# Kernel optimization log

Measured on AMD Instinct MI355X. Metric: run time of the kernel, lower is better.

## Reference

```python
import jax, jax.numpy as jnp
import numpy as np

GAMMA = 0.25  # channel_gamma


def q_shift(x, h, w, gamma=GAMMA):
    # x: [B, T, C] with T == h*w; shift 4 channel groups by 1 pixel in 4 directions
    B, T, C = x.shape
    xi = x.reshape(B, h, w, C)
    c = int(C * gamma)
    g0 = jnp.pad(xi[:, :, :-1, 0:c],        ((0, 0), (0, 0), (1, 0), (0, 0)))  # right
    g1 = jnp.pad(xi[:, :, 1:, c:2 * c],     ((0, 0), (0, 0), (0, 1), (0, 0)))  # left
    g2 = jnp.pad(xi[:, :-1, :, 2 * c:3 * c], ((0, 0), (1, 0), (0, 0), (0, 0)))  # down
    g3 = jnp.pad(xi[:, 1:, :, 3 * c:4 * c],  ((0, 0), (0, 1), (0, 0), (0, 0)))  # up
    rest = xi[:, :, :, 4 * c:]
    return jnp.concatenate([g0, g1, g2, g3, rest], axis=-1).reshape(B, T, C)


def wkv(w_dec, u, k, v):
    # Numerically-stabilized RWKV WKV recurrence.
    # w_dec, u: [C]; k, v: [B, T, C] -> y: [B, T, C]
    B, T, C = k.shape
    kT = jnp.transpose(k, (1, 0, 2))  # [T, B, C]
    vT = jnp.transpose(v, (1, 0, 2))

    def step(carry, kv_t):
        p, q, o = carry  # running num/den and log-scale, each [B, C]
        kt, vt = kv_t
        no = jnp.maximum(o, u + kt)
        A = jnp.exp(o - no)
        Bf = jnp.exp(u + kt - no)
        y = (A * p + Bf * vt) / (A * q + Bf)
        no2 = jnp.maximum(w_dec + o, kt)
        A2 = jnp.exp(w_dec + o - no2)
        B2 = jnp.exp(kt - no2)
        return (A2 * p + B2 * vt, A2 * q + B2, no2), y

    init = (jnp.zeros((B, C), k.dtype), jnp.zeros((B, C), k.dtype),
            jnp.full((B, C), -1e38, k.dtype))
    _, yT = jax.lax.scan(step, init, (kT, vT))
    return jnp.transpose(yT, (1, 0, 2))


def layer_norm(x, g, b, eps=1e-5):
    mu = jnp.mean(x, axis=-1, keepdims=True)
    var = jnp.var(x, axis=-1, keepdims=True)
    return (x - mu) * jax.lax.rsqrt(var + eps) * g + b


def setup_inputs() -> dict:
    key = jax.random.key(0)
    ks = jax.random.split(key, 12)
    B, H, W, C = 16, 32, 32, 768
    T = H * W
    x = jax.random.normal(ks[0], (B, T, C), dtype=jnp.float32)
    return {
        "x": x,
        "h": H,
        "w": W,
        "spatial_decay": jax.random.normal(ks[1], (C,), jnp.float32) * 0.5,
        "spatial_first": jax.random.normal(ks[2], (C,), jnp.float32) * 0.5,
        "mix_k": jax.random.uniform(ks[3], (1, 1, C), jnp.float32),
        "mix_v": jax.random.uniform(ks[4], (1, 1, C), jnp.float32),
        "mix_r": jax.random.uniform(ks[5], (1, 1, C), jnp.float32),
        "W_k": jax.random.normal(ks[6], (C, C), jnp.float32) * 0.02,
        "W_v": jax.random.normal(ks[7], (C, C), jnp.float32) * 0.02,
        "W_r": jax.random.normal(ks[8], (C, C), jnp.float32) * 0.02,
        "W_o": jax.random.normal(ks[9], (C, C), jnp.float32) * 0.02,
        "ln_g": jnp.ones((C,), jnp.float32),
        "ln_b": jnp.zeros((C,), jnp.float32),
    }


def reference(x, h, w, spatial_decay, spatial_first, mix_k, mix_v, mix_r,
              W_k, W_v, W_r, W_o, ln_g, ln_b):
    B, T, C = x.shape
    xx = q_shift(x, h, w)
    xk = x * mix_k + xx * (1.0 - mix_k)
    xv = x * mix_v + xx * (1.0 - mix_v)
    xr = x * mix_r + xx * (1.0 - mix_r)
    k = xk @ W_k          # [B, T, C]
    v = xv @ W_v
    sr = jax.nn.sigmoid(xr @ W_r)
    y = wkv(spatial_decay / T, spatial_first / T, k, v)
    y = layer_norm(y, ln_g, ln_b)
    return (sr * y) @ W_o
```

## Files before the change

kernel.cpp:

```cpp
#include <hip/hip_runtime.h>
#include <hip/hip_bf16.h>

using bf16 = __hip_bfloat16;
typedef __attribute__((ext_vector_type(8))) __bf16 bf16x8;
typedef __attribute__((ext_vector_type(4))) float floatx4;

#define B_  16
#define T_  1024
#define C_  768
#define M_  16384

#define OFF_XK ((size_t)0)
#define OFF_XV ((size_t)25165824)
#define OFF_XR ((size_t)50331648)
#define OFF_K  ((size_t)75497472)
#define OFF_V  ((size_t)100663296)
#define OFF_SR ((size_t)125829120)
#define OFF_WT ((size_t)150994944)
#define OFF_Y  ((size_t)0)
#define OFF_Z  ((size_t)50331648)

struct __align__(16) BV8 { bf16 v[8]; };

__global__ __launch_bounds__(256) void transpose_w(
    const float* __restrict__ w0, const float* __restrict__ w1,
    const float* __restrict__ w2, const float* __restrict__ w3,
    bf16* __restrict__ wt) {
  __shared__ float tile[32][33];
  int which = blockIdx.z;
  const float* src = which == 0 ? w0 : which == 1 ? w1 : which == 2 ? w2 : w3;
  bf16* dst = wt + (size_t)which * (C_ * C_);
  int k0 = blockIdx.y * 32;
  int n0 = blockIdx.x * 32;
  int j  = threadIdx.x & 31;
  int i0 = threadIdx.x >> 5;
#pragma unroll
  for (int s = 0; s < 4; s++) {
    int i = i0 + s * 8;
    tile[i][j] = src[(size_t)(k0 + i) * C_ + n0 + j];
  }
  __syncthreads();
#pragma unroll
  for (int s = 0; s < 4; s++) {
    int i = i0 + s * 8;
    dst[(size_t)(n0 + i) * C_ + k0 + j] = __float2bfloat16(tile[j][i]);
  }
}

__global__ __launch_bounds__(256) void shift_mix(
    const float* __restrict__ x,
    const float* __restrict__ mk, const float* __restrict__ mv, const float* __restrict__ mr,
    bf16* __restrict__ xk, bf16* __restrict__ xv, bf16* __restrict__ xr) {
  int gid = blockIdx.x * 256 + threadIdx.x;
  int c8 = gid % 96;
  int bt = gid / 96;
  int b  = bt >> 10;
  int t  = bt & 1023;
  int hh = t >> 5, ww = t & 31;
  int c0 = c8 * 8;
  int g  = c8 / 24;
  int sh = hh, sw = ww;
  bool valid;
  if (g == 0)      { sw = ww - 1; valid = (ww >= 1);  }
  else if (g == 1) { sw = ww + 1; valid = (ww <= 30); }
  else if (g == 2) { sh = hh - 1; valid = (hh >= 1);  }
  else             { sh = hh + 1; valid = (hh <= 30); }
  size_t off = (size_t)bt * C_ + c0;
  float xs[8], ss[8];
  *(float4*)(xs)     = *(const float4*)(x + off);
  *(float4*)(xs + 4) = *(const float4*)(x + off + 4);
  if (valid) {
    size_t soff = (size_t)(b * 1024 + sh * 32 + sw) * C_ + c0;
    *(float4*)(ss)     = *(const float4*)(x + soff);
    *(float4*)(ss + 4) = *(const float4*)(x + soff + 4);
  } else {
#pragma unroll
    for (int j = 0; j < 8; j++) ss[j] = 0.f;
  }
  BV8 ok, ov, orr;
#pragma unroll
  for (int j = 0; j < 8; j++) {
    float xf = xs[j], sf = ss[j];
    float a  = mk[c0 + j];
    float bm = mv[c0 + j];
    float cm = mr[c0 + j];
    ok.v[j]  = __float2bfloat16(xf * a  + sf * (1.f - a));
    ov.v[j]  = __float2bfloat16(xf * bm + sf * (1.f - bm));
    orr.v[j] = __float2bfloat16(xf * cm + sf * (1.f - cm));
  }
  *(BV8*)(xk + off) = ok;
  *(BV8*)(xv + off) = ov;
  *(BV8*)(xr + off) = orr;
}

template <int MODE>
__device__ __forceinline__ void gemm_body(
    const bf16* __restrict__ A, const bf16* __restrict__ BT,
    void* __restrict__ Cout, int M, int N, int K,
    int bx, int by) {
  __shared__ bf16 As[128 * 64];
  __shared__ bf16 Bs[128 * 64];
  int tid  = threadIdx.x;
  int wave = tid >> 6, lane = tid & 63;
  int wm = (wave & 1) * 64, wn = (wave >> 1) * 64;
  size_t m0 = (size_t)by * 128, n0 = (size_t)bx * 128;

  floatx4 acc[4][4];
#pragma unroll
  for (int i = 0; i < 4; i++)
#pragma unroll
    for (int j = 0; j < 4; j++) acc[i][j] = (floatx4){0.f, 0.f, 0.f, 0.f};

  int srow[4], skk[4];
#pragma unroll
  for (int i = 0; i < 4; i++) {
    srow[i] = ((tid >> 2) + i * 64) & 127;
    skk[i]  = (tid & 3) * 8 + (i >> 1) * 32;
  }
  bf16* lA = As + tid * 8;
  bf16* lB = Bs + tid * 8;
  int fr  = lane & 15;
  int fko = (lane >> 4) * 8;

  for (int k0 = 0; k0 < K; k0 += 64) {
#pragma unroll
    for (int i = 0; i < 4; i++) {
      __builtin_amdgcn_global_load_lds(
          (const __attribute__((address_space(1))) void*)(A + (m0 + srow[i]) * (size_t)K + k0 + skk[i]),
          (__attribute__((address_space(3))) void*)(lA + i * 2048), 16, 0, 0);
      __builtin_amdgcn_global_load_lds(
          (const __attribute__((address_space(1))) void*)(BT + (n0 + srow[i]) * (size_t)K + k0 + skk[i]),
          (__attribute__((address_space(3))) void*)(lB + i * 2048), 16, 0, 0);
    }
    __syncthreads();
#pragma unroll
    for (int s = 0; s < 2; s++) {
      bf16x8 af[4], bfr[4];
#pragma unroll
      for (int mi = 0; mi < 4; mi++)
        af[mi] = *(const bf16x8*)(As + s * 4096 + (wm + mi * 16 + fr) * 32 + fko);
#pragma unroll
      for (int ni = 0; ni < 4; ni++)
        bfr[ni] = *(const bf16x8*)(Bs + s * 4096 + (wn + ni * 16 + fr) * 32 + fko);
#pragma unroll
      for (int mi = 0; mi < 4; mi++)
#pragma unroll
        for (int ni = 0; ni < 4; ni++)
          acc[mi][ni] = __builtin_amdgcn_mfma_f32_16x16x32_bf16(
              af[mi], bfr[ni], acc[mi][ni], 0, 0, 0);
    }
    __syncthreads();
  }
  int cr = (lane >> 4) * 4;
  int cc = lane & 15;
#pragma unroll
  for (int mi = 0; mi < 4; mi++)
#pragma unroll
    for (int ni = 0; ni < 4; ni++)
#pragma unroll
      for (int i = 0; i < 4; i++) {
        size_t r   = m0 + wm + mi * 16 + cr + i;
        size_t col = n0 + wn + ni * 16 + cc;
        float val = acc[mi][ni][i];
        if (MODE == 3) {
          ((float*)Cout)[r * N + col] = val;
        } else {
          if (MODE == 2) val = 1.0f / (1.0f + __expf(-val));
          ((bf16*)Cout)[r * N + col] = __float2bfloat16(val);
        }
      }
}

template <int MODE>
__global__ __launch_bounds__(256, 2) void gemm_bt(
    const bf16* __restrict__ A, const bf16* __restrict__ BT,
    void* __restrict__ Cout, int M, int N, int K) {
  gemm_body<MODE>(A, BT, Cout, M, N, K, blockIdx.x, blockIdx.y);
}

__global__ __launch_bounds__(256, 2) void gemm_kv(
    const bf16* __restrict__ A0, const bf16* __restrict__ B0, bf16* __restrict__ C0,
    const bf16* __restrict__ A1, const bf16* __restrict__ B1, bf16* __restrict__ C1,
    int M, int N, int K) {
  if (blockIdx.z == 0)
    gemm_body<1>(A0, B0, C0, M, N, K, blockIdx.x, blockIdx.y);
  else
    gemm_body<1>(A1, B1, C1, M, N, K, blockIdx.x, blockIdx.y);
}

#define SEG 32
#define SL  32
__global__ __launch_bounds__(256) void wkv_chunked(
    const bf16* __restrict__ kT, const bf16* __restrict__ vT,
    const float* __restrict__ sd, const float* __restrict__ sf,
    bf16* __restrict__ y) {
  int tid = threadIdx.x;
  int s = tid >> 3, cr = tid & 7;
  int b = blockIdx.x / 96, cg = blockIdx.x % 96;
  int c = cg * 8 + cr;
  float w = sd[c] * (1.0f / (float)T_);
  float u = sf[c] * (1.0f / (float)T_);
  size_t base = (size_t)c * M_ + b * T_ + s * SL;
  BV8 kv[4], vv8[4];
#pragma unroll
  for (int j = 0; j < 4; j++) {
    kv[j]  = *(const BV8*)(kT + base + j * 8);
    vv8[j] = *(const BV8*)(vT + base + j * 8);
  }
  float P = 0.f, Q = 0.f, O = -1e38f;
#pragma unroll
  for (int j = 0; j < 4; j++)
#pragma unroll
    for (int i = 0; i < 8; i++) {
      float kt = __bfloat162float(kv[j].v[i]);
      float vt = __bfloat162float(vv8[j].v[i]);
      float wo = w + O;
      float no = fmaxf(wo, kt);
      float A  = __expf(wo - no);
      float Bx = __expf(kt - no);
      P = A * P + Bx * vt;
      Q = A * Q + Bx;
      O = no;
    }
  __shared__ float sP[SEG][8], sQ[SEG][8], sO[SEG][8];
  sP[s][cr] = P; sQ[s][cr] = Q; sO[s][cr] = O;
  __syncthreads();
  if (s == 0) {
    float p = 0.f, q = 0.f, o = -1e38f;
    float dw = (float)SL * w;
#pragma unroll 1
    for (int t = 0; t < SEG; t++) {
      float Pp = sP[t][cr], Qq = sQ[t][cr], Oo = sO[t][cr];
      sP[t][cr] = p; sQ[t][cr] = q; sO[t][cr] = o;
      float a  = dw + o;
      float no = fmaxf(a, Oo);
      float e1 = __expf(a - no);
      float e2 = __expf(Oo - no);
      p = e1 * p + e2 * Pp;
      q = e1 * q + e2 * Qq;
      o = no;
    }
  }
  __syncthreads();
  float p = sP[s][cr], q = sQ[s][cr], o = sO[s][cr];
  bf16* yp = y + ((size_t)(b * T_ + s * SL)) * C_ + c;
#pragma unroll
  for (int j = 0; j < 4; j++)
#pragma unroll
    for (int i = 0; i < 8; i++) {
      float kt = __bfloat162float(kv[j].v[i]);
      float vt = __bfloat162float(vv8[j].v[i]);
      float uk = u + kt;
      float no = fmaxf(o, uk);
      float A  = __expf(o - no);
      float Bx = __expf(uk - no);
      yp[(size_t)(j * 8 + i) * C_] =
          __float2bfloat16(__fdividef(A * p + Bx * vt, A * q + Bx));
      float wo  = w + o;
      float no2 = fmaxf(wo, kt);
      float A2 = __expf(wo - no2);
      float B2 = __expf(kt - no2);
      p = A2 * p + B2 * vt;
      q = A2 * q + B2;
      o = no2;
    }
}

__global__ __launch_bounds__(256) void ln_sr_kernel(
    const bf16* __restrict__ y, const bf16* __restrict__ sr,
    const float* __restrict__ gg, const float* __restrict__ bb,
    bf16* __restrict__ z) {
  int rowi = blockIdx.x;
  size_t base = (size_t)rowi * C_;
  int tid = threadIdx.x;
  float v0 = __bfloat162float(y[base + tid]);
  float v1 = __bfloat162float(y[base + tid + 256]);
  float v2 = __bfloat162float(y[base + tid + 512]);
  float s  = v0 + v1 + v2;
  float s2 = v0 * v0 + v1 * v1 + v2 * v2;
#pragma unroll
  for (int off = 32; off > 0; off >>= 1) {
    s  += __shfl_down(s, off);
    s2 += __shfl_down(s2, off);
  }
  __shared__ float red[16];
  int wv = tid >> 6, ln = tid & 63;
  if (ln == 0) { red[wv] = s; red[8 + wv] = s2; }
  __syncthreads();
  if (tid == 0) {
    float ts = red[0] + red[1] + red[2] + red[3];
    float t2 = red[8] + red[9] + red[10] + red[11];
    float mu  = ts * (1.0f / (float)C_);
    float var = t2 * (1.0f / (float)C_) - mu * mu;
    red[0] = mu;
    red[1] = rsqrtf(var + 1e-5f);
  }
  __syncthreads();
  float mu = red[0], rs = red[1];
#pragma unroll
  for (int j = 0; j < 3; j++) {
    int c = tid + j * 256;
    float val = (j == 0 ? v0 : (j == 1 ? v1 : v2));
    float gn  = gg[c];
    float bn  = bb[c];
    float srf = __bfloat162float(sr[base + c]);
    z[base + c] = __float2bfloat16(((val - mu) * rs * gn + bn) * srf);
  }
}

extern "C" void kernel_launch(void* const* d_in, const int* in_sizes, int n_in,
                              void* d_out, int out_size, void* d_ws, size_t ws_size,
                              hipStream_t stream) {
  const float* x  = (const float*)d_in[0];
  const float* sd = (const float*)d_in[3];
  const float* sf = (const float*)d_in[4];
  const float* mk = (const float*)d_in[5];
  const float* mv = (const float*)d_in[6];
  const float* mr = (const float*)d_in[7];
  const float* Wk = (const float*)d_in[8];
  const float* Wv = (const float*)d_in[9];
  const float* Wr = (const float*)d_in[10];
  const float* Wo = (const float*)d_in[11];
  const float* lg = (const float*)d_in[12];
  const float* lb = (const float*)d_in[13];

  char* ws = (char*)d_ws;
  bf16* xk  = (bf16*)(ws + OFF_XK);
  bf16* xv  = (bf16*)(ws + OFF_XV);
  bf16* xr  = (bf16*)(ws + OFF_XR);
  bf16* kTb = (bf16*)(ws + OFF_K);
  bf16* vTb = (bf16*)(ws + OFF_V);
  bf16* srb = (bf16*)(ws + OFF_SR);
  bf16* wt  = (bf16*)(ws + OFF_WT);
  bf16* WkT = wt;
  bf16* WvT = wt + (size_t)C_ * C_;
  bf16* WrT = wt + (size_t)2 * C_ * C_;
  bf16* WoT = wt + (size_t)3 * C_ * C_;
  bf16* yb  = (bf16*)(ws + OFF_Y);
  bf16* zb  = (bf16*)(ws + OFF_Z);

  transpose_w<<<dim3(24, 24, 4), 256, 0, stream>>>(Wk, Wv, Wr, Wo, wt);
  shift_mix<<<(M_ * 96) / 256, 256, 0, stream>>>(x, mk, mv, mr, xk, xv, xr);

  gemm_kv<<<dim3(M_ / 128, C_ / 128, 2), 256, 0, stream>>>(
      WkT, xk, kTb, WvT, xv, vTb, C_, M_, C_);
  dim3 ggrid(C_ / 128, M_ / 128);
  gemm_bt<2><<<ggrid, 256, 0, stream>>>(xr, WrT, srb, M_, C_, C_);

  wkv_chunked<<<B_ * 96, 256, 0, stream>>>(kTb, vTb, sd, sf, yb);
  ln_sr_kernel<<<M_, 256, 0, stream>>>(yb, srb, lg, lb, zb);

  gemm_bt<3><<<ggrid, 256, 0, stream>>>(zb, WoT, (float*)d_out, M_, C_, C_);
}
```

Baseline: 305.7 us.

## Fuse prep kernels, merge sr GEMM into transposed batch, transpose-store WKV output

Merges the weight transpose and shift-mix into one launch, and folds the sigmoid(xr@Wr) GEMM into the batched k/v GEMM so it also writes channel-major output. The WKV kernel now writes y channel-major with vectorized 16-byte stores instead of strided scalar stores. A new layernorm kernel reads channel-major y and sr, computes per-token statistics, and transposes through shared memory to produce the row-major z. This cuts launch count and scattered writes, but layernorm now makes two passes over y with per-channel strided reads.

```diff
diff --git a/kernel.cpp b/kernel.cpp
--- a/kernel.cpp
+++ b/kernel.cpp
@@ -22,75 +22,79 @@
 
 struct __align__(16) BV8 { bf16 v[8]; };
 
-__global__ __launch_bounds__(256) void transpose_w(
+__global__ __launch_bounds__(256) void prep_kernel(
+    const float* __restrict__ x,
+    const float* __restrict__ mk, const float* __restrict__ mv, const float* __restrict__ mr,
     const float* __restrict__ w0, const float* __restrict__ w1,
     const float* __restrict__ w2, const float* __restrict__ w3,
+    bf16* __restrict__ xk, bf16* __restrict__ xv, bf16* __restrict__ xr,
     bf16* __restrict__ wt) {
-  __shared__ float tile[32][33];
-  int which = blockIdx.z;
-  const float* src = which == 0 ? w0 : which == 1 ? w1 : which == 2 ? w2 : w3;
-  bf16* dst = wt + (size_t)which * (C_ * C_);
-  int k0 = blockIdx.y * 32;
-  int n0 = blockIdx.x * 32;
-  int j  = threadIdx.x & 31;
-  int i0 = threadIdx.x >> 5;
-#pragma unroll
-  for (int s = 0; s < 4; s++) {
-    int i = i0 + s * 8;
-    tile[i][j] = src[(size_t)(k0 + i) * C_ + n0 + j];
-  }
-  __syncthreads();
-#pragma unroll
-  for (int s = 0; s < 4; s++) {
-    int i = i0 + s * 8;
-    dst[(size_t)(n0 + i) * C_ + k0 + j] = __float2bfloat16(tile[j][i]);
-  }
-}
-
-__global__ __launch_bounds__(256) void shift_mix(
-    const float* __restrict__ x,
-    const float* __restrict__ mk, const float* __restrict__ mv, const float* __restrict__ mr,
-    bf16* __restrict__ xk, bf16* __restrict__ xv, bf16* __restrict__ xr) {
-  int gid = blockIdx.x * 256 + threadIdx.x;
-  int c8 = gid % 96;
-  int bt = gid / 96;
-  int b  = bt >> 10;
-  int t  = bt & 1023;
-  int hh = t >> 5, ww = t & 31;
-  int c0 = c8 * 8;
-  int g  = c8 / 24;
-  int sh = hh, sw = ww;
-  bool valid;
-  if (g == 0)      { sw = ww - 1; valid = (ww >= 1);  }
-  else if (g == 1) { sw = ww + 1; valid = (ww <= 30); }
-  else if (g == 2) { sh = hh - 1; valid = (hh >= 1);  }
-  else             { sh = hh + 1; valid = (hh <= 30); }
-  size_t off = (size_t)bt * C_ + c0;
-  float xs[8], ss[8];
-  *(float4*)(xs)     = *(const float4*)(x + off);
-  *(float4*)(xs + 4) = *(const float4*)(x + off + 4);
-  if (valid) {
-    size_t soff = (size_t)(b * 1024 + sh * 32 + sw) * C_ + c0;
-    *(float4*)(ss)     = *(const float4*)(x + soff);
-    *(float4*)(ss + 4) = *(const float4*)(x + soff + 4);
+  __shared__ float tile[32 * 33];
+  int bid = blockIdx.x;
+  if (bid < 6144) {
+    int gid = bid * 256 + threadIdx.x;
+    int c8 = gid % 96;
+    int bt = gid / 96;
+    int b  = bt >> 10;
+    int t  = bt & 1023;
+    int hh = t >> 5, ww = t & 31;
+    int c0 = c8 * 8;
+    int g  = c8 / 24;
+    int sh = hh, sw = ww;
+    bool valid;
+    if (g == 0)      { sw = ww - 1; valid = (ww >= 1);  }
+    else if (g == 1) { sw = ww + 1; valid = (ww <= 30); }
+    else if (g == 2) { sh = hh - 1; valid = (hh >= 1);  }
+    else             { sh = hh + 1; valid = (hh <= 30); }
+    size_t off = (size_t)bt * C_ + c0;
+    float xs[8], ss[8];
+    *(float4*)(xs)     = *(const float4*)(x + off);
+    *(float4*)(xs + 4) = *(const float4*)(x + off + 4);
+    if (valid) {
+      size_t soff = (size_t)(b * 1024 + sh * 32 + sw) * C_ + c0;
+      *(float4*)(ss)     = *(const float4*)(x + soff);
+      *(float4*)(ss + 4) = *(const float4*)(x + soff + 4);
+    } else {
+#pragma unroll
+      for (int j = 0; j < 8; j++) ss[j] = 0.f;
+    }
+    BV8 ok, ov, orr;
+#pragma unroll
+    for (int j = 0; j < 8; j++) {
+      float xf = xs[j], sf = ss[j];
+      float a  = mk[c0 + j];
+      float bm = mv[c0 + j];
+      float cm = mr[c0 + j];
+      ok.v[j]  = __float2bfloat16(xf * a  + sf * (1.f - a));
+      ov.v[j]  = __float2bfloat16(xf * bm + sf * (1.f - bm));
+      orr.v[j] = __float2bfloat16(xf * cm + sf * (1.f - cm));
+    }
+    *(BV8*)(xk + off) = ok;
+    *(BV8*)(xv + off) = ov;
+    *(BV8*)(xr + off) = orr;
   } else {
-#pragma unroll
-    for (int j = 0; j < 8; j++) ss[j] = 0.f;
-  }
-  BV8 ok, ov, orr;
-#pragma unroll
-  for (int j = 0; j < 8; j++) {
-    float xf = xs[j], sf = ss[j];
-    float a  = mk[c0 + j];
-    float bm = mv[c0 + j];
-    float cm = mr[c0 + j];
-    ok.v[j]  = __float2bfloat16(xf * a  + sf * (1.f - a));
-    ov.v[j]  = __float2bfloat16(xf * bm + sf * (1.f - bm));
-    orr.v[j] = __float2bfloat16(xf * cm + sf * (1.f - cm));
-  }
-  *(BV8*)(xk + off) = ok;
-  *(BV8*)(xv + off) = ov;
-  *(BV8*)(xr + off) = orr;
+    int tb = bid - 6144;
+    int which = tb / 576;
+    int rem   = tb % 576;
+    int by = rem / 24, bx = rem % 24;
+    const float* src = which == 0 ? w0 : which == 1 ? w1 : which == 2 ? w2 : w3;
+    bf16* dst = wt + (size_t)which * (C_ * C_);
+    int k0 = by * 32;
+    int n0 = bx * 32;
+    int j  = threadIdx.x & 31;
+    int i0 = threadIdx.x >> 5;
+#pragma unroll
+    for (int s = 0; s < 4; s++) {
+      int i = i0 + s * 8;
+      tile[i * 33 + j] = src[(size_t)(k0 + i) * C_ + n0 + j];
+    }
+    __syncthreads();
+#pragma unroll
+    for (int s = 0; s < 4; s++) {
+      int i = i0 + s * 8;
+      dst[(size_t)(n0 + i) * C_ + k0 + j] = __float2bfloat16(tile[j * 33 + i]);
+    }
+  }
 }
 
 template <int MODE>
@@ -178,14 +182,18 @@
   gemm_body<MODE>(A, BT, Cout, M, N, K, blockIdx.x, blockIdx.y);
 }
 
-__global__ __launch_bounds__(256, 2) void gemm_kv(
+__global__ __launch_bounds__(256, 2) void gemm_mix3(
     const bf16* __restrict__ A0, const bf16* __restrict__ B0, bf16* __restrict__ C0,
     const bf16* __restrict__ A1, const bf16* __restrict__ B1, bf16* __restrict__ C1,
+    const bf16* __restrict__ A2, const bf16* __restrict__ B2, bf16* __restrict__ C2,
     int M, int N, int K) {
-  if (blockIdx.z == 0)
+  int z = blockIdx.z;
+  if (z == 0)
     gemm_body<1>(A0, B0, C0, M, N, K, blockIdx.x, blockIdx.y);
+  else if (z == 1)
+    gemm_body<1>(A1, B1, C1, M, N, K, blockIdx.x, blockIdx.y);
   else
-    gemm_body<1>(A1, B1, C1, M, N, K, blockIdx.x, blockIdx.y);
+    gemm_body<2>(A2, B2, C2, M, N, K, blockIdx.x, blockIdx.y);
 }
 
 #define SEG 32
@@ -193,7 +201,7 @@
 __global__ __launch_bounds__(256) void wkv_chunked(
     const bf16* __restrict__ kT, const bf16* __restrict__ vT,
     const float* __restrict__ sd, const float* __restrict__ sf,
-    bf16* __restrict__ y) {
+    bf16* __restrict__ yT) {
   int tid = threadIdx.x;
   int s = tid >> 3, cr = tid & 7;
   int b = blockIdx.x / 96, cg = blockIdx.x % 96;
@@ -243,7 +251,7 @@
   }
   __syncthreads();
   float p = sP[s][cr], q = sQ[s][cr], o = sO[s][cr];
-  bf16* yp = y + ((size_t)(b * T_ + s * SL)) * C_ + c;
+  BV8 yo[4];
 #pragma unroll
   for (int j = 0; j < 4; j++)
 #pragma unroll
@@ -254,8 +262,7 @@
       float no = fmaxf(o, uk);
       float A  = __expf(o - no);
       float Bx = __expf(uk - no);
-      yp[(size_t)(j * 8 + i) * C_] =
-          __float2bfloat16(__fdividef(A * p + Bx * vt, A * q + Bx));
+      yo[j].v[i] = __float2bfloat16(__fdividef(A * p + Bx * vt, A * q + Bx));
       float wo  = w + o;
       float no2 = fmaxf(wo, kt);
       float A2 = __expf(wo - no2);
@@ -264,47 +271,61 @@
       q = A2 * q + B2;
       o = no2;
     }
-}
-
-__global__ __launch_bounds__(256) void ln_sr_kernel(
-    const bf16* __restrict__ y, const bf16* __restrict__ sr,
+  bf16* yp = yT + base;
+#pragma unroll
+  for (int j = 0; j < 4; j++) *(BV8*)(yp + j * 8) = yo[j];
+}
+
+__global__ __launch_bounds__(256) void ln_srT_kernel(
+    const bf16* __restrict__ yT, const bf16* __restrict__ srT,
     const float* __restrict__ gg, const float* __restrict__ bb,
     bf16* __restrict__ z) {
-  int rowi = blockIdx.x;
-  size_t base = (size_t)rowi * C_;
   int tid = threadIdx.x;
-  float v0 = __bfloat162float(y[base + tid]);
-  float v1 = __bfloat162float(y[base + tid + 256]);
-  float v2 = __bfloat162float(y[base + tid + 512]);
-  float s  = v0 + v1 + v2;
-  float s2 = v0 * v0 + v1 * v1 + v2 * v2;
-#pragma unroll
-  for (int off = 32; off > 0; off >>= 1) {
-    s  += __shfl_down(s, off);
-    s2 += __shfl_down(s2, off);
-  }
-  __shared__ float red[16];
-  int wv = tid >> 6, ln = tid & 63;
-  if (ln == 0) { red[wv] = s; red[8 + wv] = s2; }
+  int btl = tid & 63;
+  int cs  = tid >> 6;
+  int bt0 = blockIdx.x * 64;
+  int bt  = bt0 + btl;
+  float s = 0.f, s2 = 0.f;
+#pragma unroll 4
+  for (int i = 0; i < 192; i++) {
+    int c = cs * 192 + i;
+    float v = __bfloat162float(yT[(size_t)c * M_ + bt]);
+    s += v; s2 += v * v;
+  }
+  __shared__ float rs_[4][64], r2_[4][64];
+  rs_[cs][btl] = s; r2_[cs][btl] = s2;
   __syncthreads();
-  if (tid == 0) {
-    float ts = red[0] + red[1] + red[2] + red[3];
-    float t2 = red[8] + red[9] + red[10] + red[11];
+  __shared__ float mu_[64], sig_[64];
+  if (tid < 64) {
+    float ts = rs_[0][tid] + rs_[1][tid] + rs_[2][tid] + rs_[3][tid];
+    float t2 = r2_[0][tid] + r2_[1][tid] + r2_[2][tid] + r2_[3][tid];
     float mu  = ts * (1.0f / (float)C_);
     float var = t2 * (1.0f / (float)C_) - mu * mu;
-    red[0] = mu;
-    red[1] = rsqrtf(var + 1e-5f);
+    mu_[tid]  = mu;
+    sig_[tid] = rsqrtf(var + 1e-5f);
   }
   __syncthreads();
-  float mu = red[0], rs = red[1];
-#pragma unroll
-  for (int j = 0; j < 3; j++) {
-    int c = tid + j * 256;
-    float val = (j == 0 ? v0 : (j == 1 ? v1 : v2));
-    float gn  = gg[c];
-    float bn  = bb[c];
-    float srf = __bfloat162float(sr[base + c]);
-    z[base + c] = __float2bfloat16(((val - mu) * rs * gn + bn) * srf);
+  float mu = mu_[btl], rs = sig_[btl];
+  __shared__ bf16 tile[64 * 72];
+  for (int ch = 0; ch < 12; ch++) {
+    int cbase = ch * 64;
+#pragma unroll
+    for (int i = 0; i < 16; i++) {
+      int c = cbase + cs * 16 + i;
+      float v  = __bfloat162float(yT[(size_t)c * M_ + bt]);
+      float sr = __bfloat162float(srT[(size_t)c * M_ + bt]);
+      float zv = ((v - mu) * rs * gg[c] + bb[c]) * sr;
+      tile[btl * 72 + cs * 16 + i] = __float2bfloat16(zv);
+    }
+    __syncthreads();
+#pragma unroll
+    for (int sw = 0; sw < 2; sw++) {
+      int r  = (tid >> 3) + sw * 32;
+      int cc = (tid & 7) * 8;
+      BV8 val = *(const BV8*)&tile[r * 72 + cc];
+      *(BV8*)(z + (size_t)(bt0 + r) * C_ + cbase + cc) = val;
+    }
+    __syncthreads();
   }
 }
 
@@ -330,25 +351,24 @@
   bf16* xr  = (bf16*)(ws + OFF_XR);
   bf16* kTb = (bf16*)(ws + OFF_K);
   bf16* vTb = (bf16*)(ws + OFF_V);
-  bf16* srb = (bf16*)(ws + OFF_SR);
+  bf16* srT = (bf16*)(ws + OFF_SR);
   bf16* wt  = (bf16*)(ws + OFF_WT);
   bf16* WkT = wt;
   bf16* WvT = wt + (size_t)C_ * C_;
   bf16* WrT = wt + (size_t)2 * C_ * C_;
   bf16* WoT = wt + (size_t)3 * C_ * C_;
-  bf16* yb  = (bf16*)(ws + OFF_Y);
+  bf16* yTb = (bf16*)(ws + OFF_Y);
   bf16* zb  = (bf16*)(ws + OFF_Z);
 
-  transpose_w<<<dim3(24, 24, 4), 256, 0, stream>>>(Wk, Wv, Wr, Wo, wt);
-  shift_mix<<<(M_ * 96) / 256, 256, 0, stream>>>(x, mk, mv, mr, xk, xv, xr);
-
-  gemm_kv<<<dim3(M_ / 128, C_ / 128, 2), 256, 0, stream>>>(
-      WkT, xk, kTb, WvT, xv, vTb, C_, M_, C_);
-  dim3 ggrid(C_ / 128, M_ / 128);
-  gemm_bt<2><<<ggrid, 256, 0, stream>>>(xr, WrT, srb, M_, C_, C_);
-
-  wkv_chunked<<<B_ * 96, 256, 0, stream>>>(kTb, vTb, sd, sf, yb);
-  ln_sr_kernel<<<M_, 256, 0, stream>>>(yb, srb, lg, lb, zb);
-
-  gemm_bt<3><<<ggrid, 256, 0, stream>>>(zb, WoT, (float*)d_out, M_, C_, C_);
-}
+  prep_kernel<<<8448, 256, 0, stream>>>(x, mk, mv, mr, Wk, Wv, Wr, Wo,
+                                        xk, xv, xr, wt);
+
+  gemm_mix3<<<dim3(M_ / 128, C_ / 128, 3), 256, 0, stream>>>(
+      WkT, xk, kTb, WvT, xv, vTb, WrT, xr, srT, C_, M_, C_);
+
+  wkv_chunked<<<B_ * 96, 256, 0, stream>>>(kTb, vTb, sd, sf, yTb);
+  ln_srT_kernel<<<M_ / 64, 256, 0, stream>>>(yTb, srT, lg, lb, zb);
+
+  gemm_bt<3><<<dim3(C_ / 128, M_ / 128), 256, 0, stream>>>(
+      zb, WoT, (float*)d_out, M_, C_, C_);
+}
```

After: 345.3 us. 1.13x slower.
